# Kernel tuning notes

Measured on AMD Instinct MI355X. Metric: run time of the kernel, lower is better.

Reference implementation:

```python
import jax, jax.numpy as jnp
import numpy as np

N_NODES = 20000
N_EDGES = 80000
D = 128       # in_dim_node == in_dim_edge == hidden dims
ITERS = 15    # mp_iterations
EPS = 1e-5    # torch LayerNorm default eps


def _mlp(h, W0, b0, W1, b1, W2, b2, gamma, beta):
    """Linear-ReLU-Linear-ReLU-Linear-LayerNorm (hidden_layers=2)."""
    h = jax.nn.relu(h @ W0 + b0)
    h = jax.nn.relu(h @ W1 + b1)
    h = h @ W2 + b2
    mu = jnp.mean(h, axis=-1, keepdims=True)
    var = jnp.var(h, axis=-1, keepdims=True)
    return gamma * (h - mu) * jax.lax.rsqrt(var + EPS) + beta


def setup_inputs() -> dict:
    key = jax.random.key(0)
    ks = iter(jax.random.split(key, 32))

    def lin(fi, fo):
        bnd = 1.0 / np.sqrt(fi)
        W = jax.random.uniform(next(ks), (ITERS, fi, fo), minval=-bnd, maxval=bnd, dtype=jnp.float32)
        b = jax.random.uniform(next(ks), (ITERS, fo), minval=-bnd, maxval=bnd, dtype=jnp.float32)
        return W, b

    x = jax.random.normal(next(ks), (N_NODES, D), dtype=jnp.float32)
    edge_attr = jax.random.normal(next(ks), (N_EDGES, D), dtype=jnp.float32)
    edge_index = jax.random.randint(next(ks), (2, N_EDGES), 0, N_NODES)

    eW0, eB0 = lin(3 * D, D)   # edge MLP input = cat(src, dest, edge) = 384
    eW1, eB1 = lin(D, D)
    eW2, eB2 = lin(D, D)
    nW0, nB0 = lin(2 * D, D)   # node MLP input = cat(x, agg) = 256
    nW1, nB1 = lin(D, D)
    nW2, nB2 = lin(D, D)
    ones = jnp.ones((ITERS, D), jnp.float32)
    zeros = jnp.zeros((ITERS, D), jnp.float32)

    return dict(x=x, edge_attr=edge_attr,
                eW0=eW0, eB0=eB0, eW1=eW1, eB1=eB1, eW2=eW2, eB2=eB2, eG=ones, eBeta=zeros,
                nW0=nW0, nB0=nB0, nW1=nW1, nB1=nB1, nW2=nW2, nB2=nB2, nG=ones, nBeta=zeros,
                edge_index=edge_index)


def reference(x, edge_attr, eW0, eB0, eW1, eB1, eW2, eB2, eG, eBeta,
              nW0, nB0, nW1, nB1, nW2, nB2, nG, nBeta, edge_index):
    row, col = edge_index[0], edge_index[1]
    n = x.shape[0]
    params = (eW0, eB0, eW1, eB1, eW2, eB2, eG, eBeta,
              nW0, nB0, nW1, nB1, nW2, nB2, nG, nBeta)

    def step(carry, p):
        xc, ec = carry
        (ew0, eb0, ew1, eb1, ew2, eb2, eg, ebt,
         nw0, nb0, nw1, nb1, nw2, nb2, ng, nbt) = p
        # EdgeProcessor: gather + MLP, then FullResidualConnection (add previous)
        e_in = jnp.concatenate([xc[row], xc[col], ec], axis=-1)        # [E, 3D]
        ec = _mlp(e_in, ew0, eb0, ew1, eb1, ew2, eb2, eg, ebt) + ec
        # NodeProcessor: scatter_sum over destination nodes + MLP + residual
        agg = jax.ops.segment_sum(ec, col, num_segments=n)             # [N, D]
        n_in = jnp.concatenate([xc, agg], axis=-1)                     # [N, 2D]
        xc = _mlp(n_in, nw0, nb0, nw1, nb1, nw2, nb2, ng, nbt) + xc
        return (xc, ec), None

    (x, edge_attr), _ = jax.lax.scan(step, (x, edge_attr), params)
    return x, edge_attr
```

## Files before the change

### kernel.cpp

```cpp
#include <hip/hip_runtime.h>
#include <hip/hip_bf16.h>

typedef __hip_bfloat16 bf16;
typedef __attribute__((ext_vector_type(8))) short short8;
typedef __attribute__((ext_vector_type(4))) float f32x4;

#define NN 20000
#define NE 80000
#define DD 128
#define NITER 15
#define HSTRIDE 136

__device__ inline void gload16(const void* g, void* l) {
  __builtin_amdgcn_global_load_lds(
      (const __attribute__((address_space(1))) void*)g,
      (__attribute__((address_space(3))) void*)l, 16, 0, 0);
}

__global__ void detect_kernel(const unsigned short* __restrict__ p, int nhalf,
                              int* __restrict__ flag) {
  __shared__ int cs[256], ct[256];
  const int t = threadIdx.x;
  int sane = 0, tot = 0;
  for (int i = 2 * t; i < nhalf; i += 512) {
    unsigned short v = p[i];
    int e = (v >> 7) & 0xFF;
    tot++;
    if (v == 0 || (e >= 80 && e <= 170)) sane++;
  }
  cs[t] = sane; ct[t] = tot;
  __syncthreads();
  for (int o = 128; o > 0; o >>= 1) {
    if (t < o) { cs[t] += cs[t + o]; ct[t] += ct[t + o]; }
    __syncthreads();
  }
  if (t == 0) *flag = (cs[0] * 10 > ct[0] * 7) ? 1 : 0;
}

__global__ void in2fb_kernel(const void* __restrict__ src, float* __restrict__ dstf,
                             bf16* __restrict__ dstb, int n, const int* __restrict__ flag) {
  int i = blockIdx.x * 256 + threadIdx.x;
  if (i < n) {
    float v = (*flag) ? (float)((const bf16*)src)[i] : ((const float*)src)[i];
    dstf[i] = v;
    dstb[i] = (bf16)v;
  }
}

__global__ void in2f_kernel(const void* __restrict__ src, float* __restrict__ dst,
                            int n, const int* __restrict__ flag) {
  int i = blockIdx.x * 256 + threadIdx.x;
  if (i < n) {
    dst[i] = (*flag) ? (float)((const bf16*)src)[i] : ((const float*)src)[i];
  }
}

__global__ void w2t_kernel(const void* __restrict__ W, bf16* __restrict__ Wt,
                           int K, const int* __restrict__ flag) {
  int i = blockIdx.x * 256 + threadIdx.x;
  int total = NITER * K * DD;
  if (i < total) {
    float v = (*flag) ? (float)((const bf16*)W)[i] : ((const float*)W)[i];
    int t = i / (K * DD);
    int rem = i - t * K * DD;
    int k = rem >> 7;
    int n = rem & 127;
    Wt[(size_t)t * K * DD + (size_t)n * K + k] = (bf16)v;
  }
}

__global__ void outw_kernel(const float* __restrict__ xf, const float* __restrict__ ef,
                            void* __restrict__ out, const int* __restrict__ flag) {
  int i = blockIdx.x * 256 + threadIdx.x;
  const int nx = NN * DD, total = (NN + NE) * DD;
  if (i < total) {
    float v = (i < nx) ? xf[i] : ef[i - nx];
    if (*flag) ((bf16*)out)[i] = (bf16)v;
    else       ((float*)out)[i] = v;
  }
}

template<int K0, int AMODE>
__global__ __launch_bounds__(256, 3) void fused_mlp(
    const bf16*  __restrict__ S0b,
    const bf16*  __restrict__ S1b,
    const int*   __restrict__ eidx,
    const bf16*  __restrict__ W0t,
    const bf16*  __restrict__ W1t,
    const bf16*  __restrict__ W2t,
    const float* __restrict__ b0,
    const float* __restrict__ b1,
    const float* __restrict__ b2,
    const float* __restrict__ gamma,
    const float* __restrict__ beta,
    float*       __restrict__ stf,
    bf16*        __restrict__ stb,
    int M)
{
  __shared__ __align__(16) bf16 Bls[128 * 32];
  __shared__ __align__(16) bf16 Hls[128 * HSTRIDE];

  const int tid  = threadIdx.x;
  const int lane = tid & 63;
  const int wv   = tid >> 6;
  const int l15  = lane & 15, quad = lane >> 4;
  const int m0   = blockIdx.x * 128;

  const int scol = tid >> 2;
  const int sk8  = (tid & 3) * 8;

  int rowm[2], ir[2], ic[2];
#pragma unroll
  for (int mi = 0; mi < 2; mi++) {
    rowm[mi] = min(m0 + wv * 32 + mi * 16 + l15, M - 1);
    if (AMODE == 1) { ir[mi] = eidx[rowm[mi]]; ic[mi] = eidx[NE + rowm[mi]]; }
  }

  f32x4 acc[2][8];
#pragma unroll
  for (int i = 0; i < 2; i++)
#pragma unroll
    for (int j = 0; j < 8; j++) acc[i][j] = (f32x4){0.f, 0.f, 0.f, 0.f};

#pragma unroll
  for (int s = 0; s < K0 / 32; s++) {
    const int kk = s * 32;
    __syncthreads();
    gload16(W0t + (size_t)scol * K0 + kk + sk8,        &Bls[scol * 32 + sk8]);
    gload16(W0t + (size_t)(scol + 64) * K0 + kk + sk8, &Bls[(scol + 64) * 32 + sk8]);
    short8 af[2];
    {
      const int ks = (kk & 127) + quad * 8;
#pragma unroll
      for (int mi = 0; mi < 2; mi++) {
        const bf16* base;
        if (AMODE == 1) {
          const int seg = kk >> 7;
          base = (seg == 0) ? S0b + (size_t)ir[mi] * DD
               : (seg == 1) ? S0b + (size_t)ic[mi] * DD
                            : S1b + (size_t)rowm[mi] * DD;
        } else {
          base = (kk >> 7) ? S1b + (size_t)rowm[mi] * DD
                           : S0b + (size_t)rowm[mi] * DD;
        }
        af[mi] = *(const short8*)(base + ks);
      }
    }
    __syncthreads();
    short8 bfr[8];
#pragma unroll
    for (int ni = 0; ni < 8; ni++)
      bfr[ni] = *(const short8*)&Bls[(ni * 16 + l15) * 32 + quad * 8];
#pragma unroll
    for (int mi = 0; mi < 2; mi++)
#pragma unroll
      for (int ni = 0; ni < 8; ni++)
        acc[mi][ni] = __builtin_amdgcn_mfma_f32_16x16x32_bf16(af[mi], bfr[ni], acc[mi][ni], 0, 0, 0);
  }
  {
    float bv[8];
#pragma unroll
    for (int ni = 0; ni < 8; ni++) bv[ni] = b0[ni * 16 + l15];
#pragma unroll
    for (int mi = 0; mi < 2; mi++)
#pragma unroll
      for (int r = 0; r < 4; r++) {
        const int row = wv * 32 + mi * 16 + quad * 4 + r;
#pragma unroll
        for (int ni = 0; ni < 8; ni++)
          Hls[row * HSTRIDE + ni * 16 + l15] = (bf16)fmaxf(acc[mi][ni][r] + bv[ni], 0.f);
      }
  }

#pragma unroll
  for (int i = 0; i < 2; i++)
#pragma unroll
    for (int j = 0; j < 8; j++) acc[i][j] = (f32x4){0.f, 0.f, 0.f, 0.f};
#pragma unroll
  for (int s = 0; s < 4; s++) {
    const int kk = s * 32;
    __syncthreads();
    gload16(W1t + (size_t)scol * 128 + kk + sk8,        &Bls[scol * 32 + sk8]);
    gload16(W1t + (size_t)(scol + 64) * 128 + kk + sk8, &Bls[(scol + 64) * 32 + sk8]);
    __syncthreads();
    short8 af[2], bfr[8];
#pragma unroll
    for (int mi = 0; mi < 2; mi++)
      af[mi] = *(const short8*)&Hls[(wv * 32 + mi * 16 + l15) * HSTRIDE + kk + quad * 8];
#pragma unroll
    for (int ni = 0; ni < 8; ni++)
      bfr[ni] = *(const short8*)&Bls[(ni * 16 + l15) * 32 + quad * 8];
#pragma unroll
    for (int mi = 0; mi < 2; mi++)
#pragma unroll
      for (int ni = 0; ni < 8; ni++)
        acc[mi][ni] = __builtin_amdgcn_mfma_f32_16x16x32_bf16(af[mi], bfr[ni], acc[mi][ni], 0, 0, 0);
  }
  __syncthreads();
  {
    float bv[8];
#pragma unroll
    for (int ni = 0; ni < 8; ni++) bv[ni] = b1[ni * 16 + l15];
#pragma unroll
    for (int mi = 0; mi < 2; mi++)
#pragma unroll
      for (int r = 0; r < 4; r++) {
        const int row = wv * 32 + mi * 16 + quad * 4 + r;
#pragma unroll
        for (int ni = 0; ni < 8; ni++)
          Hls[row * HSTRIDE + ni * 16 + l15] = (bf16)fmaxf(acc[mi][ni][r] + bv[ni], 0.f);
      }
  }

#pragma unroll
  for (int i = 0; i < 2; i++)
#pragma unroll
    for (int j = 0; j < 8; j++) acc[i][j] = (f32x4){0.f, 0.f, 0.f, 0.f};
#pragma unroll
  for (int s = 0; s < 4; s++) {
    const int kk = s * 32;
    __syncthreads();
    gload16(W2t + (size_t)scol * 128 + kk + sk8,        &Bls[scol * 32 + sk8]);
    gload16(W2t + (size_t)(scol + 64) * 128 + kk + sk8, &Bls[(scol + 64) * 32 + sk8]);
    __syncthreads();
    short8 af[2], bfr[8];
#pragma unroll
    for (int mi = 0; mi < 2; mi++)
      af[mi] = *(const short8*)&Hls[(wv * 32 + mi * 16 + l15) * HSTRIDE + kk + quad * 8];
#pragma unroll
    for (int ni = 0; ni < 8; ni++)
      bfr[ni] = *(const short8*)&Bls[(ni * 16 + l15) * 32 + quad * 8];
#pragma unroll
    for (int mi = 0; mi < 2; mi++)
#pragma unroll
      for (int ni = 0; ni < 8; ni++)
        acc[mi][ni] = __builtin_amdgcn_mfma_f32_16x16x32_bf16(af[mi], bfr[ni], acc[mi][ni], 0, 0, 0);
  }

  float bv[8], gv[8], btv[8];
#pragma unroll
  for (int ni = 0; ni < 8; ni++) {
    const int col = ni * 16 + l15;
    bv[ni] = b2[col]; gv[ni] = gamma[col]; btv[ni] = beta[col];
  }
#pragma unroll
  for (int mi = 0; mi < 2; mi++)
#pragma unroll
    for (int r = 0; r < 4; r++) {
      float a = 0.f, bq = 0.f;
#pragma unroll
      for (int ni = 0; ni < 8; ni++) {
        const float v = acc[mi][ni][r] + bv[ni];
        a += v; bq += v * v;
      }
#pragma unroll
      for (int off = 1; off < 16; off <<= 1) {
        a  += __shfl_xor(a, off);
        bq += __shfl_xor(bq, off);
      }
      const float mu = a * (1.0f / 128.0f);
      const float var = fmaxf(bq * (1.0f / 128.0f) - mu * mu, 0.0f);
      const float rs = rsqrtf(var + 1e-5f);
      const int m = m0 + wv * 32 + mi * 16 + quad * 4 + r;
      if (m < M) {
#pragma unroll
        for (int ni = 0; ni < 8; ni++) {
          const int col = ni * 16 + l15;
          const float v = acc[mi][ni][r] + bv[ni];
          const float lnv = (v - mu) * rs * gv[ni] + btv[ni];
          const size_t idx = (size_t)m * DD + col;
          const float nv = lnv + stf[idx];
          stf[idx] = nv;
          stb[idx] = (bf16)nv;
        }
      }
    }
}

__global__ void zero_kernel(int* __restrict__ p, int n) {
  int i = blockIdx.x * 256 + threadIdx.x;
  if (i < n) p[i] = 0;
}

__global__ void hist_kernel(const int* __restrict__ eidx, int* __restrict__ counts) {
  int e = blockIdx.x * 256 + threadIdx.x;
  if (e < NE) atomicAdd(&counts[eidx[NE + e]], 1);
}

__global__ void scan_kernel(const int* __restrict__ counts, int* __restrict__ offs,
                            int* __restrict__ cursor) {
  __shared__ int sums[1024];
  const int t = threadIdx.x;
  const int base = t * 20;
  int local[20];
  int s = 0;
  for (int i = 0; i < 20; i++) {
    int idx = base + i;
    int c = (idx < NN) ? counts[idx] : 0;
    local[i] = s; s += c;
  }
  sums[t] = s;
  __syncthreads();
  for (int off = 1; off < 1024; off <<= 1) {
    int v = 0;
    if (t >= off) v = sums[t - off];
    __syncthreads();
    if (t >= off) sums[t] += v;
    __syncthreads();
  }
  int excl = (t == 0) ? 0 : sums[t - 1];
  for (int i = 0; i < 20; i++) {
    int idx = base + i;
    if (idx < NN) { offs[idx] = excl + local[i]; cursor[idx] = 0; }
  }
  if (t == 1023) offs[NN] = sums[1023];
}

__global__ void fill_kernel(const int* __restrict__ eidx, const int* __restrict__ offs,
                            int* __restrict__ cursor, int* __restrict__ sorted) {
  int e = blockIdx.x * 256 + threadIdx.x;
  if (e < NE) {
    int n = eidx[NE + e];
    int p = atomicAdd(&cursor[n], 1);
    sorted[offs[n] + p] = e;
  }
}

__global__ void aggregate_kernel(const bf16* __restrict__ eb, const int* __restrict__ offs,
                                 const int* __restrict__ sorted, bf16* __restrict__ aggb) {
  const int node = blockIdx.x * 4 + (threadIdx.x >> 6);
  const int lane = threadIdx.x & 63;
  if (node >= NN) return;
  const int s = offs[node], t = offs[node + 1];
  float a0 = 0.f, a1 = 0.f;
  for (int i = s; i < t; i++) {
    const int e = sorted[i];
    a0 += (float)eb[(size_t)e * DD + lane];
    a1 += (float)eb[(size_t)e * DD + 64 + lane];
  }
  aggb[(size_t)node * DD + lane]      = (bf16)a0;
  aggb[(size_t)node * DD + 64 + lane] = (bf16)a1;
}

extern "C" void kernel_launch(void* const* d_in, const int* in_sizes, int n_in,
                              void* d_out, int out_size, void* d_ws, size_t ws_size,
                              hipStream_t stream) {
  const void* x_in = d_in[0];
  const void* e_in = d_in[1];
  const void* eW0 = d_in[2];
  const void* eB0 = d_in[3];
  const void* eW1 = d_in[4];
  const void* eB1 = d_in[5];
  const void* eW2 = d_in[6];
  const void* eB2 = d_in[7];
  const void* eG  = d_in[8];
  const void* eBt = d_in[9];
  const void* nW0 = d_in[10];
  const void* nB0 = d_in[11];
  const void* nW1 = d_in[12];
  const void* nB1 = d_in[13];
  const void* nW2 = d_in[14];
  const void* nB2 = d_in[15];
  const void* nG  = d_in[16];
  const void* nBt = d_in[17];
  const int*  eidx = (const int*)d_in[18];

  char* ws = (char*)d_ws;
  size_t off = 0;
  auto alloc = [&](size_t bytes) -> char* {
    char* p = ws + off;
    off = (off + bytes + 255) & ~(size_t)255;
    return p;
  };

  float* xf   = (float*)alloc((size_t)NN * DD * 4);
  float* ef   = (float*)alloc((size_t)NE * DD * 4);
  bf16*  xb   = (bf16*)alloc((size_t)NN * DD * 2);
  bf16*  eb   = (bf16*)alloc((size_t)NE * DD * 2);
  bf16*  aggb = (bf16*)alloc((size_t)NN * DD * 2);
  bf16*  eW0t = (bf16*)alloc((size_t)NITER * 384 * DD * 2);
  bf16*  eW1t = (bf16*)alloc((size_t)NITER * 128 * DD * 2);
  bf16*  eW2t = (bf16*)alloc((size_t)NITER * 128 * DD * 2);
  bf16*  nW0t = (bf16*)alloc((size_t)NITER * 256 * DD * 2);
  bf16*  nW1t = (bf16*)alloc((size_t)NITER * 128 * DD * 2);
  bf16*  nW2t = (bf16*)alloc((size_t)NITER * 128 * DD * 2);
  const int NB = NITER * DD;
  float* eB0f = (float*)alloc(NB * 4);
  float* eB1f = (float*)alloc(NB * 4);
  float* eB2f = (float*)alloc(NB * 4);
  float* eGf  = (float*)alloc(NB * 4);
  float* eBtf = (float*)alloc(NB * 4);
  float* nB0f = (float*)alloc(NB * 4);
  float* nB1f = (float*)alloc(NB * 4);
  float* nB2f = (float*)alloc(NB * 4);
  float* nGf  = (float*)alloc(NB * 4);
  float* nBtf = (float*)alloc(NB * 4);
  int* counts = (int*)alloc((size_t)NN * 4);
  int* cursor = (int*)alloc((size_t)NN * 4);
  int* offs   = (int*)alloc((size_t)(NN + 1) * 4);
  int* sorted = (int*)alloc((size_t)NE * 4);
  int* flag   = (int*)alloc(4);

  detect_kernel<<<1, 256, 0, stream>>>((const unsigned short*)x_in, 16384, flag);

  in2fb_kernel<<<(NN * DD + 255) / 256, 256, 0, stream>>>(x_in, xf, xb, NN * DD, flag);
  in2fb_kernel<<<(NE * DD + 255) / 256, 256, 0, stream>>>(e_in, ef, eb, NE * DD, flag);
  w2t_kernel<<<(NITER * 384 * DD + 255) / 256, 256, 0, stream>>>(eW0, eW0t, 384, flag);
  w2t_kernel<<<(NITER * 128 * DD + 255) / 256, 256, 0, stream>>>(eW1, eW1t, 128, flag);
  w2t_kernel<<<(NITER * 128 * DD + 255) / 256, 256, 0, stream>>>(eW2, eW2t, 128, flag);
  w2t_kernel<<<(NITER * 256 * DD + 255) / 256, 256, 0, stream>>>(nW0, nW0t, 256, flag);
  w2t_kernel<<<(NITER * 128 * DD + 255) / 256, 256, 0, stream>>>(nW1, nW1t, 128, flag);
  w2t_kernel<<<(NITER * 128 * DD + 255) / 256, 256, 0, stream>>>(nW2, nW2t, 128, flag);
  in2f_kernel<<<(NB + 255) / 256, 256, 0, stream>>>(eB0, eB0f, NB, flag);
  in2f_kernel<<<(NB + 255) / 256, 256, 0, stream>>>(eB1, eB1f, NB, flag);
  in2f_kernel<<<(NB + 255) / 256, 256, 0, stream>>>(eB2, eB2f, NB, flag);
  in2f_kernel<<<(NB + 255) / 256, 256, 0, stream>>>(eG,  eGf,  NB, flag);
  in2f_kernel<<<(NB + 255) / 256, 256, 0, stream>>>(eBt, eBtf, NB, flag);
  in2f_kernel<<<(NB + 255) / 256, 256, 0, stream>>>(nB0, nB0f, NB, flag);
  in2f_kernel<<<(NB + 255) / 256, 256, 0, stream>>>(nB1, nB1f, NB, flag);
  in2f_kernel<<<(NB + 255) / 256, 256, 0, stream>>>(nB2, nB2f, NB, flag);
  in2f_kernel<<<(NB + 255) / 256, 256, 0, stream>>>(nG,  nGf,  NB, flag);
  in2f_kernel<<<(NB + 255) / 256, 256, 0, stream>>>(nBt, nBtf, NB, flag);

  zero_kernel<<<(NN + 255) / 256, 256, 0, stream>>>(counts, NN);
  hist_kernel<<<(NE + 255) / 256, 256, 0, stream>>>(eidx, counts);
  scan_kernel<<<1, 1024, 0, stream>>>(counts, offs, cursor);
  fill_kernel<<<(NE + 255) / 256, 256, 0, stream>>>(eidx, offs, cursor, sorted);

  const int egrid = NE / 128;
  const int ngrid = (NN + 127) / 128;

  for (int t = 0; t < NITER; t++) {
    fused_mlp<384, 1><<<egrid, 256, 0, stream>>>(
        xb, eb, eidx,
        eW0t + (size_t)t * 384 * DD, eW1t + (size_t)t * 128 * DD, eW2t + (size_t)t * 128 * DD,
        eB0f + t * DD, eB1f + t * DD, eB2f + t * DD,
        eGf + t * DD, eBtf + t * DD, ef, eb, NE);
    aggregate_kernel<<<(NN + 3) / 4, 256, 0, stream>>>(eb, offs, sorted, aggb);
    fused_mlp<256, 2><<<ngrid, 256, 0, stream>>>(
        xb, aggb, nullptr,
        nW0t + (size_t)t * 256 * DD, nW1t + (size_t)t * 128 * DD, nW2t + (size_t)t * 128 * DD,
        nB0f + t * DD, nB1f + t * DD, nB2f + t * DD,
        nGf + t * DD, nBtf + t * DD, xf, xb, NN);
  }

  outw_kernel<<<((NN + NE) * DD + 255) / 256, 256, 0, stream>>>(xf, ef, d_out, flag);
}
```

Before: 1.294 ms.

## Double-buffer weight slabs across MLP layers and vectorize aggregation loads

Doubles the LDS weight-slab buffer so the DMA for the next K-slab, including the first slab of the next layer, is issued before the MFMAs on the current slab. This removes one barrier per slab and overlaps weight loads with compute. The A-row gather for the first layer is also software-pipelined one slab ahead. Separately, the aggregation kernel now reads and writes two bf16 values per lane with 32-bit accesses and converts them by bit shifting. The extra LDS buffer raises shared memory per block and may reduce occupancy.

```diff
diff --git a/kernel.cpp b/kernel.cpp
--- a/kernel.cpp
+++ b/kernel.cpp
@@ -15,6 +15,10 @@
   __builtin_amdgcn_global_load_lds(
       (const __attribute__((address_space(1))) void*)g,
       (__attribute__((address_space(3))) void*)l, 16, 0, 0);
+}
+
+__device__ inline float bfbits2f(unsigned int hi16) {
+  union { unsigned int u; float f; } c; c.u = hi16; return c.f;
 }
 
 __global__ void detect_kernel(const unsigned short* __restrict__ p, int nhalf,
@@ -97,7 +101,7 @@
     bf16*        __restrict__ stb,
     int M)
 {
-  __shared__ __align__(16) bf16 Bls[128 * 32];
+  __shared__ __align__(16) bf16 Bls[2][128 * 32];
   __shared__ __align__(16) bf16 Hls[128 * HSTRIDE];
 
   const int tid  = threadIdx.x;
@@ -116,51 +120,64 @@
     if (AMODE == 1) { ir[mi] = eidx[rowm[mi]]; ic[mi] = eidx[NE + rowm[mi]]; }
   }
 
+  auto dmaW = [&](const bf16* W, int K, int kk, int buf) {
+    gload16(W + (size_t)scol * K + kk + sk8,        &Bls[buf][scol * 32 + sk8]);
+    gload16(W + (size_t)(scol + 64) * K + kk + sk8, &Bls[buf][(scol + 64) * 32 + sk8]);
+  };
+  auto gatherA = [&](int kk, short8 a[2]) {
+    const int ks = (kk & 127) + quad * 8;
+#pragma unroll
+    for (int mi = 0; mi < 2; mi++) {
+      const bf16* base;
+      if (AMODE == 1) {
+        const int seg = kk >> 7;
+        base = (seg == 0) ? S0b + (size_t)ir[mi] * DD
+             : (seg == 1) ? S0b + (size_t)ic[mi] * DD
+                          : S1b + (size_t)rowm[mi] * DD;
+      } else {
+        base = (kk >> 7) ? S1b + (size_t)rowm[mi] * DD
+                         : S0b + (size_t)rowm[mi] * DD;
+      }
+      a[mi] = *(const short8*)(base + ks);
+    }
+  };
+
   f32x4 acc[2][8];
-#pragma unroll
-  for (int i = 0; i < 2; i++)
-#pragma unroll
-    for (int j = 0; j < 8; j++) acc[i][j] = (f32x4){0.f, 0.f, 0.f, 0.f};
-
-#pragma unroll
-  for (int s = 0; s < K0 / 32; s++) {
-    const int kk = s * 32;
-    __syncthreads();
-    gload16(W0t + (size_t)scol * K0 + kk + sk8,        &Bls[scol * 32 + sk8]);
-    gload16(W0t + (size_t)(scol + 64) * K0 + kk + sk8, &Bls[(scol + 64) * 32 + sk8]);
-    short8 af[2];
-    {
-      const int ks = (kk & 127) + quad * 8;
-#pragma unroll
-      for (int mi = 0; mi < 2; mi++) {
-        const bf16* base;
-        if (AMODE == 1) {
-          const int seg = kk >> 7;
-          base = (seg == 0) ? S0b + (size_t)ir[mi] * DD
-               : (seg == 1) ? S0b + (size_t)ic[mi] * DD
-                            : S1b + (size_t)rowm[mi] * DD;
-        } else {
-          base = (kk >> 7) ? S1b + (size_t)rowm[mi] * DD
-                           : S0b + (size_t)rowm[mi] * DD;
-        }
-        af[mi] = *(const short8*)(base + ks);
-      }
-    }
-    __syncthreads();
+  auto zacc = [&]() {
+#pragma unroll
+    for (int i = 0; i < 2; i++)
+#pragma unroll
+      for (int j = 0; j < 8; j++) acc[i][j] = (f32x4){0.f, 0.f, 0.f, 0.f};
+  };
+  auto slabMfmaA = [&](const short8 a[2], int buf) {
     short8 bfr[8];
 #pragma unroll
     for (int ni = 0; ni < 8; ni++)
-      bfr[ni] = *(const short8*)&Bls[(ni * 16 + l15) * 32 + quad * 8];
+      bfr[ni] = *(const short8*)&Bls[buf][(ni * 16 + l15) * 32 + quad * 8];
 #pragma unroll
     for (int mi = 0; mi < 2; mi++)
 #pragma unroll
       for (int ni = 0; ni < 8; ni++)
-        acc[mi][ni] = __builtin_amdgcn_mfma_f32_16x16x32_bf16(af[mi], bfr[ni], acc[mi][ni], 0, 0, 0);
-  }
-  {
+        acc[mi][ni] = __builtin_amdgcn_mfma_f32_16x16x32_bf16(a[mi], bfr[ni], acc[mi][ni], 0, 0, 0);
+  };
+  auto slabMfmaH = [&](int kk, int buf) {
+    short8 a[2], bfr[8];
+#pragma unroll
+    for (int mi = 0; mi < 2; mi++)
+      a[mi] = *(const short8*)&Hls[(wv * 32 + mi * 16 + l15) * HSTRIDE + kk + quad * 8];
+#pragma unroll
+    for (int ni = 0; ni < 8; ni++)
+      bfr[ni] = *(const short8*)&Bls[buf][(ni * 16 + l15) * 32 + quad * 8];
+#pragma unroll
+    for (int mi = 0; mi < 2; mi++)
+#pragma unroll
+      for (int ni = 0; ni < 8; ni++)
+        acc[mi][ni] = __builtin_amdgcn_mfma_f32_16x16x32_bf16(a[mi], bfr[ni], acc[mi][ni], 0, 0, 0);
+  };
+  auto writeH = [&](const float* bias) {
     float bv[8];
 #pragma unroll
-    for (int ni = 0; ni < 8; ni++) bv[ni] = b0[ni * 16 + l15];
+    for (int ni = 0; ni < 8; ni++) bv[ni] = bias[ni * 16 + l15];
 #pragma unroll
     for (int mi = 0; mi < 2; mi++)
 #pragma unroll
@@ -170,71 +187,47 @@
         for (int ni = 0; ni < 8; ni++)
           Hls[row * HSTRIDE + ni * 16 + l15] = (bf16)fmaxf(acc[mi][ni][r] + bv[ni], 0.f);
       }
-  }
-
-#pragma unroll
-  for (int i = 0; i < 2; i++)
-#pragma unroll
-    for (int j = 0; j < 8; j++) acc[i][j] = (f32x4){0.f, 0.f, 0.f, 0.f};
+  };
+
+  constexpr int NS1 = K0 / 32;
+
+  zacc();
+  short8 aCur[2], aNxt[2];
+  dmaW(W0t, K0, 0, 0);
+  gatherA(0, aCur);
+  __syncthreads();
+#pragma unroll
+  for (int s = 0; s < NS1; s++) {
+    if (s + 1 < NS1) {
+      dmaW(W0t, K0, (s + 1) * 32, (s + 1) & 1);
+      gatherA((s + 1) * 32, aNxt);
+    } else {
+      dmaW(W1t, 128, 0, NS1 & 1);
+    }
+    slabMfmaA(aCur, s & 1);
+    __syncthreads();
+    aCur[0] = aNxt[0]; aCur[1] = aNxt[1];
+  }
+  writeH(b0);
+  __syncthreads();
+
+  zacc();
 #pragma unroll
   for (int s = 0; s < 4; s++) {
-    const int kk = s * 32;
+    if (s < 3) dmaW(W1t, 128, (s + 1) * 32, (NS1 + s + 1) & 1);
+    else       dmaW(W2t, 128, 0,            (NS1 + 4) & 1);
+    slabMfmaH(s * 32, (NS1 + s) & 1);
     __syncthreads();
-    gload16(W1t + (size_t)scol * 128 + kk + sk8,        &Bls[scol * 32 + sk8]);
-    gload16(W1t + (size_t)(scol + 64) * 128 + kk + sk8, &Bls[(scol + 64) * 32 + sk8]);
-    __syncthreads();
-    short8 af[2], bfr[8];
-#pragma unroll
-    for (int mi = 0; mi < 2; mi++)
-      af[mi] = *(const short8*)&Hls[(wv * 32 + mi * 16 + l15) * HSTRIDE + kk + quad * 8];
-#pragma unroll
-    for (int ni = 0; ni < 8; ni++)
-      bfr[ni] = *(const short8*)&Bls[(ni * 16 + l15) * 32 + quad * 8];
-#pragma unroll
-    for (int mi = 0; mi < 2; mi++)
-#pragma unroll
-      for (int ni = 0; ni < 8; ni++)
-        acc[mi][ni] = __builtin_amdgcn_mfma_f32_16x16x32_bf16(af[mi], bfr[ni], acc[mi][ni], 0, 0, 0);
-  }
+  }
+  writeH(b1);
   __syncthreads();
-  {
-    float bv[8];
-#pragma unroll
-    for (int ni = 0; ni < 8; ni++) bv[ni] = b1[ni * 16 + l15];
-#pragma unroll
-    for (int mi = 0; mi < 2; mi++)
-#pragma unroll
-      for (int r = 0; r < 4; r++) {
-        const int row = wv * 32 + mi * 16 + quad * 4 + r;
-#pragma unroll
-        for (int ni = 0; ni < 8; ni++)
-          Hls[row * HSTRIDE + ni * 16 + l15] = (bf16)fmaxf(acc[mi][ni][r] + bv[ni], 0.f);
-      }
-  }
-
-#pragma unroll
-  for (int i = 0; i < 2; i++)
-#pragma unroll
-    for (int j = 0; j < 8; j++) acc[i][j] = (f32x4){0.f, 0.f, 0.f, 0.f};
+
+  zacc();
 #pragma unroll
   for (int s = 0; s < 4; s++) {
-    const int kk = s * 32;
-    __syncthreads();
-    gload16(W2t + (size_t)scol * 128 + kk + sk8,        &Bls[scol * 32 + sk8]);
-    gload16(W2t + (size_t)(scol + 64) * 128 + kk + sk8, &Bls[(scol + 64) * 32 + sk8]);
-    __syncthreads();
-    short8 af[2], bfr[8];
-#pragma unroll
-    for (int mi = 0; mi < 2; mi++)
-      af[mi] = *(const short8*)&Hls[(wv * 32 + mi * 16 + l15) * HSTRIDE + kk + quad * 8];
-#pragma unroll
-    for (int ni = 0; ni < 8; ni++)
-      bfr[ni] = *(const short8*)&Bls[(ni * 16 + l15) * 32 + quad * 8];
-#pragma unroll
-    for (int mi = 0; mi < 2; mi++)
-#pragma unroll
-      for (int ni = 0; ni < 8; ni++)
-        acc[mi][ni] = __builtin_amdgcn_mfma_f32_16x16x32_bf16(af[mi], bfr[ni], acc[mi][ni], 0, 0, 0);
+    if (s < 3) dmaW(W2t, 128, (s + 1) * 32, (NS1 + 4 + s + 1) & 1);
+    slabMfmaH(s * 32, (NS1 + 4 + s) & 1);
+    if (s < 3) __syncthreads();
   }
 
   float bv[8], gv[8], btv[8];
@@ -335,11 +328,14 @@
   float a0 = 0.f, a1 = 0.f;
   for (int i = s; i < t; i++) {
     const int e = sorted[i];
-    a0 += (float)eb[(size_t)e * DD + lane];
-    a1 += (float)eb[(size_t)e * DD + 64 + lane];
-  }
-  aggb[(size_t)node * DD + lane]      = (bf16)a0;
-  aggb[(size_t)node * DD + 64 + lane] = (bf16)a1;
+    unsigned int v = *(const unsigned int*)(eb + (size_t)e * DD + 2 * lane);
+    a0 += bfbits2f(v << 16);
+    a1 += bfbits2f(v & 0xFFFF0000u);
+  }
+  bf16 o0 = (bf16)a0, o1 = (bf16)a1;
+  unsigned int pack = (unsigned int)(*(unsigned short*)&o0)
+                    | ((unsigned int)(*(unsigned short*)&o1) << 16);
+  *(unsigned int*)(aggb + (size_t)node * DD + 2 * lane) = pack;
 }
 
 extern "C" void kernel_launch(void* const* d_in, const int* in_sizes, int n_in,
```

After: 1.295 ms. No clear change (+0.1%).
